# Kernel tuning notes

Hardware: AMD Instinct MI355X
Metric: run time of the kernel (lower is better)

The kernel has to match this reference:

```python
import jax, jax.numpy as jnp
import numpy as np

K, M, NUM_HOM = 32, 16, 2
B, N = 32, 2048
EPS = 1e-12


def _safe_norm(x):
    # stable L2 norm over last axis, keepdims
    return jnp.sqrt(jnp.sum(x * x, axis=-1, keepdims=True) + EPS)


def setup_inputs() -> dict:
    key = jax.random.key(0)
    k1, k2, k3, k4, k5 = jax.random.split(key, 5)
    pts = jax.random.normal(k1, (B, N, M), jnp.float32)
    hom = jax.random.randint(k2, (B, N), 0, NUM_HOM).astype(jnp.float32)
    dgm = jnp.concatenate([hom[..., None], pts], axis=-1)  # [B,N,M+1]
    # ragged diagrams: zero-pad a suffix per batch element; the original
    # while-loop stops at the first all-zero row (count_nonzero == 0)
    lengths = jax.random.randint(k3, (B,), N // 2, N + 1)
    mask = (jnp.arange(N)[None, :] < lengths[:, None]).astype(jnp.float32)
    dgm = dgm * mask[..., None]
    theta = 0.05 * jax.random.normal(k4, (K, M), jnp.float32)
    class_w = 0.05 * jax.random.normal(k5, (NUM_HOM,), jnp.float32)
    return {"dgm": dgm, "theta": theta, "class_w": class_w}


def reference(dgm, theta, class_w):
    # dgm: [B,N,M+1]; col 0 = homology class, cols 1: = embedded point
    hom = dgm[..., 0].astype(jnp.int32)  # [B,N]
    y = dgm[..., 1:]                      # [B,N,M]
    # while-loop validity: hom <= 1 AND row not all-zero; early exit -> prefix mask
    valid_pt = (hom <= 1) & jnp.any(dgm != 0, axis=-1)
    valid = jnp.cumprod(valid_pt.astype(dgm.dtype), axis=1)  # [B,N]
    w = class_w[jnp.clip(hom, 0, class_w.shape[0] - 1)] * valid  # [B,N]
    # Poincare parametrization: scale by theta_k, map R^m -> ball (hyperboloid chart)
    u = y[:, :, None, :] * theta[None, None, :, :]  # [B,N,K,M]
    un = _safe_norm(u)
    x = u / (1.0 + jnp.sqrt(1.0 + un * un))         # ||x|| < 1
    # log map at origin x_o = 0, c = 1: atanh(||x||) * x/||x||
    xn = _safe_norm(x)
    t = jnp.arctanh(jnp.clip(xn, 0.0, 1.0 - 1e-5)) * x / xn  # [B,N,K,M]
    # weighted segment sum over points; note: `sum` in the original is NOT
    # reset between k iterations -> cumulative sum over bases k
    S = jnp.einsum('bn,bnkm->bkm', w, t)
    S = jnp.cumsum(S, axis=1)  # [B,K,M]
    # exp map at origin (c=1): tanh(||v||) * v/||v||
    Sn = _safe_norm(S)
    xd = jnp.tanh(Sn) * S / Sn
    # chart back to R^m (inverse of the ball parametrization)
    xdn2 = jnp.sum(xd * xd, axis=-1, keepdims=True)
    yd = 2.0 * xd / jnp.maximum(1.0 - xdn2, 1e-7)
    return yd.reshape(dgm.shape[0], K * M)
```

## Files before the change

### kernel.cpp

```cpp
#include <hip/hip_runtime.h>
#include <math.h>

#define B_ 32
#define N_ 2048
#define M_ 16
#define K_ 32
#define EPS 1e-12f

constexpr int NC      = 128;
constexpr int NCHUNK  = N_ / NC;
constexpr int THREADS = 256;
constexpr int YSTRIDE = 20;
constexpr int SLICE64 = K_ * M_ / 2;
constexpr unsigned FLAG_TAG = 0xA5B1u;

__device__ __forceinline__ float fast_atanh(float x) {
    float ratio = (1.0f + x) * __builtin_amdgcn_rcpf(1.0f - x);
    return 0.34657359f * __log2f(ratio);
}

__global__ __launch_bounds__(THREADS) void pml_fused_kernel(
    const float* __restrict__ dgm, const float* __restrict__ theta,
    const float* __restrict__ class_w,
    unsigned long long* __restrict__ G_part,
    unsigned* __restrict__ done,
    unsigned* __restrict__ elect,
    float* __restrict__ out)
{
    __shared__ __align__(16) float y_lds[NC * YSTRIDE];
    __shared__ float hom_lds[NC];
    __shared__ float w_lds[NC];
    __shared__ unsigned wred[2];
    __shared__ float red[4][K_ * (M_ + 1)];
    __shared__ float S_lds[K_ * M_];
    __shared__ unsigned fl_lds[NCHUNK];
    __shared__ int win;

    const int b    = blockIdx.y;
    const int c    = blockIdx.x;
    const int tid  = threadIdx.x;
    const int k    = tid & (K_ - 1);
    const int grp  = tid >> 5;
    const int lane = tid & 63;
    const int wv   = tid >> 6;

    const float4* src4 = (const float4*)(dgm + ((size_t)b * N_ + c * NC) * (M_ + 1));
    for (int i4 = tid; i4 < NC * (M_ + 1) / 4; i4 += THREADS) {
        float4 v = src4[i4];
        int i  = i4 * 4;
        int nl = i / (M_ + 1);
        int j  = i - nl * (M_ + 1);
        float vv[4] = { v.x, v.y, v.z, v.w };
#pragma unroll
        for (int e = 0; e < 4; ++e) {
            if (j == 0) hom_lds[nl] = vv[e];
            else        y_lds[nl * YSTRIDE + (j - 1)] = vv[e];
            if (++j == M_ + 1) { j = 0; ++nl; }
        }
    }
    __syncthreads();

    const float cw0 = class_w[0], cw1 = class_w[1];
    if (tid < NC) {
        const float4* yv = (const float4*)(y_lds + tid * YSTRIDE);
        float4 a0 = yv[0], a1 = yv[1], a2 = yv[2], a3 = yv[3];
        float  h  = hom_lds[tid];
        bool nz = (h != 0.0f) |
                  (a0.x != 0.0f) | (a0.y != 0.0f) | (a0.z != 0.0f) | (a0.w != 0.0f) |
                  (a1.x != 0.0f) | (a1.y != 0.0f) | (a1.z != 0.0f) | (a1.w != 0.0f) |
                  (a2.x != 0.0f) | (a2.y != 0.0f) | (a2.z != 0.0f) | (a2.w != 0.0f) |
                  (a3.x != 0.0f) | (a3.y != 0.0f) | (a3.z != 0.0f) | (a3.w != 0.0f);
        bool ok = ((int)h <= 1) && nz;
        unsigned long long bal = __ballot(!ok);
        if (lane == 0)
            wred[wv] = bal ? (unsigned)(wv * 64 + (__ffsll((long long)bal) - 1))
                           : 0xFFFFFFFFu;
        int hc = min(max((int)h, 0), 1);
        w_lds[tid] = hc ? cw1 : cw0;
    }
    __syncthreads();
    const int local_mn = (int)min(min(wred[0], wred[1]), (unsigned)NC);

    float t2[M_];
#pragma unroll
    for (int m = 0; m < M_; ++m) { float t = theta[k * M_ + m]; t2[m] = t * t; }
    float g[M_];
#pragma unroll
    for (int m = 0; m < M_; ++m) g[m] = 0.0f;

    for (int nl = grp; nl < local_mn; nl += 8) {
        float w = w_lds[nl];
        const float4* yv = (const float4*)(y_lds + nl * YSTRIDE);
        float4 a0 = yv[0], a1 = yv[1], a2 = yv[2], a3 = yv[3];
        float y[M_] = { a0.x, a0.y, a0.z, a0.w,  a1.x, a1.y, a1.z, a1.w,
                        a2.x, a2.y, a2.z, a2.w,  a3.x, a3.y, a3.z, a3.w };
        float s = 0.0f;
#pragma unroll
        for (int m = 0; m < M_; ++m) s = fmaf(y[m] * y[m], t2[m], s);
        float d   = 1.0f + sqrtf(1.0f + s + EPS);
        float rd  = __builtin_amdgcn_rcpf(d);
        float xn2 = fmaf(s, rd * rd, EPS);
        float xn  = sqrtf(xn2);
        float inv_xnd = __builtin_amdgcn_rsqf(xn2) * rd;
        float xc  = fminf(xn, 1.0f - 1e-5f);
        float wc  = w * (fast_atanh(xc) * inv_xnd);
#pragma unroll
        for (int m = 0; m < M_; ++m) g[m] = fmaf(wc, y[m], g[m]);
    }

#pragma unroll
    for (int m = 0; m < M_; ++m) g[m] += __shfl_down(g[m], 32, 64);
    if (lane < K_) {
#pragma unroll
        for (int m = 0; m < M_; ++m) red[wv][lane * (M_ + 1) + m] = g[m];
    }
    __syncthreads();

    unsigned long long* dst = G_part + ((size_t)b * NCHUNK + c) * SLICE64;
    {
        int p  = tid;
        int kk = p >> 3, mp = (p & 7) * 2;
        int i0 = kk * (M_ + 1) + mp;
        float v0 = red[0][i0] + red[1][i0] + red[2][i0] + red[3][i0];
        float v1 = red[0][i0+1] + red[1][i0+1] + red[2][i0+1] + red[3][i0+1];
        unsigned long long pk =
            ((unsigned long long)__float_as_uint(v1) << 32) | __float_as_uint(v0);
        __hip_atomic_exchange(dst + p, pk, __ATOMIC_RELAXED,
                              __HIP_MEMORY_SCOPE_AGENT);
    }
    asm volatile("s_waitcnt vmcnt(0)" ::: "memory");
    __syncthreads();

    if (tid == 0) {
        __hip_atomic_exchange(&done[b * NCHUNK + c],
                              (FLAG_TAG << 16) | (unsigned)local_mn,
                              __ATOMIC_RELAXED, __HIP_MEMORY_SCOPE_AGENT);
        asm volatile("s_waitcnt vmcnt(0)" ::: "memory");
    }
    __syncthreads();

    if (tid < NCHUNK)
        fl_lds[tid] = __hip_atomic_fetch_add(&done[b * NCHUNK + tid], 0u,
                                             __ATOMIC_RELAXED,
                                             __HIP_MEMORY_SCOPE_AGENT);
    __syncthreads();

    bool allset = true;
#pragma unroll
    for (int cc = 0; cc < NCHUNK; ++cc) {
        unsigned v = fl_lds[cc];
        if ((v >> 16) != FLAG_TAG || (v & 0xFFFFu) > (unsigned)NC) allset = false;
    }
    if (!allset) return;

    if (tid == 0) {
        unsigned old = __hip_atomic_exchange(&elect[b], (FLAG_TAG << 16) | 1u,
                                             __ATOMIC_RELAXED,
                                             __HIP_MEMORY_SCOPE_AGENT);
        win = ((old >> 16) != FLAG_TAG);
    }
    __syncthreads();
    if (!win) return;

    int ninc = NCHUNK;
    for (int cc = 0; cc < NCHUNK; ++cc) {
        if ((fl_lds[cc] & 0xFFFFu) < (unsigned)NC) { ninc = cc + 1; break; }
    }

    unsigned long long* Gb = G_part + (size_t)b * NCHUNK * SLICE64;
    {
        int p  = tid;
        float s0 = 0.0f, s1 = 0.0f;
        for (int cc = 0; cc < ninc; ++cc) {
            unsigned long long pk = __hip_atomic_fetch_add(
                &Gb[cc * SLICE64 + p], 0ULL,
                __ATOMIC_RELAXED, __HIP_MEMORY_SCOPE_AGENT);
            s0 += __uint_as_float((unsigned)pk);
            s1 += __uint_as_float((unsigned)(pk >> 32));
        }
        int kk = p >> 3, mp = (p & 7) * 2;
        S_lds[kk * M_ + mp]     = s0;
        S_lds[kk * M_ + mp + 1] = s1;
    }
    __syncthreads();

    if (tid < K_) {
        const int klane = tid;
        float S[M_];
#pragma unroll
        for (int m = 0; m < M_; ++m)
            S[m] = theta[klane * M_ + m] * S_lds[klane * M_ + m];

#pragma unroll
        for (int m = 0; m < M_; ++m) {
            float v = S[m];
#pragma unroll
            for (int off = 1; off < K_; off <<= 1) {
                float up = __shfl_up(v, off, 32);
                if (klane >= off) v += up;
            }
            S[m] = v;
        }

        float sn2 = 0.0f;
#pragma unroll
        for (int m = 0; m < M_; ++m) sn2 = fmaf(S[m], S[m], sn2);
        float Sn = sqrtf(sn2 + EPS);
        float e2 = __expf(-2.0f * Sn);
        float r  = (1.0f - e2) * __builtin_amdgcn_rcpf((1.0f + e2) * Sn);

        float xd[M_];
        float xdn2 = 0.0f;
#pragma unroll
        for (int m = 0; m < M_; ++m) { xd[m] = r * S[m]; xdn2 = fmaf(xd[m], xd[m], xdn2); }
        float scale = 2.0f / fmaxf(1.0f - xdn2, 1e-7f);

#pragma unroll
        for (int m = 0; m < M_; ++m)
            out[(size_t)b * (K_ * M_) + klane * M_ + m] = scale * xd[m];
    }
}

extern "C" void kernel_launch(void* const* d_in, const int* in_sizes, int n_in,
                              void* d_out, int out_size, void* d_ws, size_t ws_size,
                              hipStream_t stream) {
    const float* dgm     = (const float*)d_in[0];
    const float* theta   = (const float*)d_in[1];
    const float* class_w = (const float*)d_in[2];
    float* out = (float*)d_out;

    unsigned long long* G_part = (unsigned long long*)d_ws;
    unsigned* done  = (unsigned*)((char*)d_ws +
                      (size_t)B_ * NCHUNK * SLICE64 * sizeof(unsigned long long));
    unsigned* elect = done + B_ * NCHUNK;

    dim3 grid(NCHUNK, B_);
    pml_fused_kernel<<<grid, THREADS, 0, stream>>>(dgm, theta, class_w,
                                                   G_part, done, elect, out);
}
```

Baseline: 73.15 us.

## Halve chunk size and use plain atomic loads/stores for cross-block reduction

Chunks shrink from 128 to 64 points, so the grid doubles to 32 blocks per batch row and each block's valid-prefix detection uses a single wavefront ballot. Partial-sum publication and flag polling switch from atomic exchange and fetch_add(0) to relaxed atomic stores and loads, which avoid read-modify-write traffic. The partial-sum gather is moved before the election exchange so it can overlap the elect atomic. The cost is a larger cross-block reduction, with twice as many partial slices and flags to write and read.

```diff
diff --git a/kernel.cpp b/kernel.cpp
--- a/kernel.cpp
+++ b/kernel.cpp
@@ -7,10 +7,11 @@
 #define K_ 32
 #define EPS 1e-12f
 
-constexpr int NC      = 128;
+constexpr int NC      = 64;
 constexpr int NCHUNK  = N_ / NC;
 constexpr int THREADS = 256;
 constexpr int YSTRIDE = 20;
+constexpr int F4      = NC * (M_ + 1) / 4;
 constexpr int SLICE64 = K_ * M_ / 2;
 constexpr unsigned FLAG_TAG = 0xA5B1u;
 
@@ -30,7 +31,7 @@
     __shared__ __align__(16) float y_lds[NC * YSTRIDE];
     __shared__ float hom_lds[NC];
     __shared__ float w_lds[NC];
-    __shared__ unsigned wred[2];
+    __shared__ unsigned wred0;
     __shared__ float red[4][K_ * (M_ + 1)];
     __shared__ float S_lds[K_ * M_];
     __shared__ unsigned fl_lds[NCHUNK];
@@ -45,7 +46,7 @@
     const int wv   = tid >> 6;
 
     const float4* src4 = (const float4*)(dgm + ((size_t)b * N_ + c * NC) * (M_ + 1));
-    for (int i4 = tid; i4 < NC * (M_ + 1) / 4; i4 += THREADS) {
+    for (int i4 = tid; i4 < F4; i4 += THREADS) {
         float4 v = src4[i4];
         int i  = i4 * 4;
         int nl = i / (M_ + 1);
@@ -72,14 +73,13 @@
                   (a3.x != 0.0f) | (a3.y != 0.0f) | (a3.z != 0.0f) | (a3.w != 0.0f);
         bool ok = ((int)h <= 1) && nz;
         unsigned long long bal = __ballot(!ok);
-        if (lane == 0)
-            wred[wv] = bal ? (unsigned)(wv * 64 + (__ffsll((long long)bal) - 1))
-                           : 0xFFFFFFFFu;
+        if (tid == 0)
+            wred0 = bal ? (unsigned)(__ffsll((long long)bal) - 1) : 0xFFFFFFFFu;
         int hc = min(max((int)h, 0), 1);
         w_lds[tid] = hc ? cw1 : cw0;
     }
     __syncthreads();
-    const int local_mn = (int)min(min(wred[0], wred[1]), (unsigned)NC);
+    const int local_mn = (int)min(wred0, (unsigned)NC);
 
     float t2[M_];
 #pragma unroll
@@ -118,31 +118,30 @@
 
     unsigned long long* dst = G_part + ((size_t)b * NCHUNK + c) * SLICE64;
     {
-        int p  = tid;
-        int kk = p >> 3, mp = (p & 7) * 2;
+        int kk = tid >> 3, mp = (tid & 7) * 2;
         int i0 = kk * (M_ + 1) + mp;
         float v0 = red[0][i0] + red[1][i0] + red[2][i0] + red[3][i0];
         float v1 = red[0][i0+1] + red[1][i0+1] + red[2][i0+1] + red[3][i0+1];
         unsigned long long pk =
             ((unsigned long long)__float_as_uint(v1) << 32) | __float_as_uint(v0);
-        __hip_atomic_exchange(dst + p, pk, __ATOMIC_RELAXED,
-                              __HIP_MEMORY_SCOPE_AGENT);
+        __hip_atomic_store(dst + tid, pk, __ATOMIC_RELAXED,
+                           __HIP_MEMORY_SCOPE_AGENT);
     }
     asm volatile("s_waitcnt vmcnt(0)" ::: "memory");
     __syncthreads();
 
     if (tid == 0) {
-        __hip_atomic_exchange(&done[b * NCHUNK + c],
-                              (FLAG_TAG << 16) | (unsigned)local_mn,
-                              __ATOMIC_RELAXED, __HIP_MEMORY_SCOPE_AGENT);
+        __hip_atomic_store(&done[b * NCHUNK + c],
+                           (FLAG_TAG << 16) | (unsigned)local_mn,
+                           __ATOMIC_RELAXED, __HIP_MEMORY_SCOPE_AGENT);
         asm volatile("s_waitcnt vmcnt(0)" ::: "memory");
     }
     __syncthreads();
 
     if (tid < NCHUNK)
-        fl_lds[tid] = __hip_atomic_fetch_add(&done[b * NCHUNK + tid], 0u,
-                                             __ATOMIC_RELAXED,
-                                             __HIP_MEMORY_SCOPE_AGENT);
+        fl_lds[tid] = __hip_atomic_load(&done[b * NCHUNK + tid],
+                                        __ATOMIC_RELAXED,
+                                        __HIP_MEMORY_SCOPE_AGENT);
     __syncthreads();
 
     bool allset = true;
@@ -152,6 +151,23 @@
         if ((v >> 16) != FLAG_TAG || (v & 0xFFFFu) > (unsigned)NC) allset = false;
     }
     if (!allset) return;
+
+    int ninc = NCHUNK;
+#pragma unroll
+    for (int cc = 0; cc < NCHUNK; ++cc) {
+        if ((fl_lds[cc] & 0xFFFFu) < (unsigned)NC) { ninc = cc + 1; break; }
+    }
+    float s0 = 0.0f, s1 = 0.0f;
+    {
+        const unsigned long long* Gb = G_part + (size_t)b * NCHUNK * SLICE64;
+        for (int cc = 0; cc < ninc; ++cc) {
+            unsigned long long pk = __hip_atomic_load(&Gb[cc * SLICE64 + tid],
+                                                      __ATOMIC_RELAXED,
+                                                      __HIP_MEMORY_SCOPE_AGENT);
+            s0 += __uint_as_float((unsigned)pk);
+            s1 += __uint_as_float((unsigned)(pk >> 32));
+        }
+    }
 
     if (tid == 0) {
         unsigned old = __hip_atomic_exchange(&elect[b], (FLAG_TAG << 16) | 1u,
@@ -162,23 +178,8 @@
     __syncthreads();
     if (!win) return;
 
-    int ninc = NCHUNK;
-    for (int cc = 0; cc < NCHUNK; ++cc) {
-        if ((fl_lds[cc] & 0xFFFFu) < (unsigned)NC) { ninc = cc + 1; break; }
-    }
-
-    unsigned long long* Gb = G_part + (size_t)b * NCHUNK * SLICE64;
     {
-        int p  = tid;
-        float s0 = 0.0f, s1 = 0.0f;
-        for (int cc = 0; cc < ninc; ++cc) {
-            unsigned long long pk = __hip_atomic_fetch_add(
-                &Gb[cc * SLICE64 + p], 0ULL,
-                __ATOMIC_RELAXED, __HIP_MEMORY_SCOPE_AGENT);
-            s0 += __uint_as_float((unsigned)pk);
-            s1 += __uint_as_float((unsigned)(pk >> 32));
-        }
-        int kk = p >> 3, mp = (p & 7) * 2;
+        int kk = tid >> 3, mp = (tid & 7) * 2;
         S_lds[kk * M_ + mp]     = s0;
         S_lds[kk * M_ + mp + 1] = s1;
     }
```

Result: slower. 77.35 us (+5.7%).
